# Kernel optimization log

Measured on AMD Instinct MI355X. Metric: run time of the kernel, lower is better.

Reference implementation:

```python
import jax, jax.numpy as jnp
import numpy as np

N = 100_000        # nodes
E = 1_600_000      # edges (avg degree 16)
IN_DIM = 256
OUT_DIM = 32
HEADS = 4
EDGE_DIM = 64
NUM_ETYPES = 8
NEG_SLOPE = 0.2


def setup_inputs() -> dict:
    key = jax.random.key(0)
    ks = jax.random.split(key, 12)
    h = jax.random.normal(ks[0], (N, IN_DIM), dtype=jnp.float32)
    row = jax.random.randint(ks[1], (E,), 0, N, dtype=jnp.int32)
    col = jax.random.randint(ks[2], (E,), 0, N, dtype=jnp.int32)
    etype = jax.random.randint(ks[3], (E,), 0, NUM_ETYPES, dtype=jnp.int32)
    # learned parameters (xavier-ish scale)
    W = jax.random.normal(ks[4], (IN_DIM, OUT_DIM * HEADS), dtype=jnp.float32) * 0.08
    edge_emb = jax.random.normal(ks[5], (NUM_ETYPES, EDGE_DIM), dtype=jnp.float32) * 0.2
    Wr = jax.random.normal(ks[6], (NUM_ETYPES, EDGE_DIM, EDGE_DIM * HEADS), dtype=jnp.float32) * 0.1
    a_l = jax.random.normal(ks[7], (1, HEADS, OUT_DIM), dtype=jnp.float32) * 0.3
    a_r = jax.random.normal(ks[8], (1, HEADS, OUT_DIM), dtype=jnp.float32) * 0.3
    a_e = jax.random.normal(ks[9], (1, HEADS, EDGE_DIM), dtype=jnp.float32) * 0.3
    res_W = jax.random.normal(ks[10], (IN_DIM, OUT_DIM * HEADS), dtype=jnp.float32) * 0.08
    res_b = jnp.zeros((OUT_DIM * HEADS,), dtype=jnp.float32)
    return dict(h=h, W=W, edge_emb=edge_emb, Wr=Wr, a_l=a_l, a_r=a_r, a_e=a_e,
                res_W=res_W, res_b=res_b, row=row, col=col, etype=etype)


def reference(h, W, edge_emb, Wr, a_l, a_r, a_e, res_W, res_b, row, col, etype):
    n = h.shape[0]
    heads, out_dim = a_l.shape[1], a_l.shape[2]
    edge_dim = a_e.shape[2]
    n_etypes = edge_emb.shape[0]

    # node transform: [N, H, D]
    emb = (h @ W).reshape(n, heads, out_dim)
    emb = jnp.where(jnp.isnan(emb), 0.0, emb)

    # typed linear on edge-type embeddings; only num_etypes distinct rows,
    # so compute per type then gather per edge (same math as W_r(edge_emb[etype]))
    e_trans = jnp.einsum('te,tef->tf', edge_emb, Wr).reshape(n_etypes, heads, edge_dim)
    h_e_type = (a_e * e_trans).sum(-1)            # [T, H]

    h_l = (a_l * emb).sum(-1)                     # [N, H]
    h_r = (a_r * emb).sum(-1)                     # [N, H]

    att = h_l[row] + h_r[col] + h_e_type[etype]   # [E, H]
    att = jnp.where(att > 0, att, NEG_SLOPE * att)  # leaky relu

    # edge softmax grouped by destination node (col)
    seg_max = jax.ops.segment_max(att, col, num_segments=n)   # [N, H]
    ex = jnp.exp(att - seg_max[col])
    seg_sum = jax.ops.segment_sum(ex, col, num_segments=n)    # [N, H]
    alpha = ex / seg_sum[col]                                  # [E, H]

    # u_mul_e + sum aggregation; emb permuted to [N, D, H] as in the original
    emb_p = emb.transpose(0, 2, 1)                 # [N, D, H]
    msg = emb_p[row] * alpha[:, None, :]           # [E, D, H]
    agg = jax.ops.segment_sum(msg, col, num_segments=n)  # [N, D, H]
    h_out = agg.reshape(n, out_dim * heads)

    h_out = h_out + h @ res_W + res_b              # residual linear
    return jax.nn.elu(h_out)
```

## Files before the change

### kernel.cpp

```cpp
#include <hip/hip_runtime.h>
#include <hip/hip_bf16.h>
#include <math.h>

#define N_NODES   100000
#define N_EDGES   1600000
#define IN_DIM    256
#define OUT_DIM   32
#define HEADS     4
#define C_DIM     128
#define EDGE_DIM  64
#define NUM_ETY   8
#define NEG_SLOPE 0.2f
#define NBLK_SCAN 391
#define M_TILE    128
#define BSTRIDE   40

typedef __attribute__((ext_vector_type(8))) short s8b;
typedef __attribute__((ext_vector_type(4))) float f32x4;
typedef unsigned short ushort_t;

__device__ __forceinline__ short bfc(float x) {
    __hip_bfloat16 b = __float2bfloat16(x);
    return *reinterpret_cast<short*>(&b);
}

__global__ void kz_init(unsigned int* __restrict__ counts) {
    int i = blockIdx.x * blockDim.x + threadIdx.x;
    if (i < N_NODES) counts[i] = 0u;
}

__global__ __launch_bounds__(256) void k_het(
    const float* __restrict__ edge_emb, const float* __restrict__ Wr,
    const float* __restrict__ a_e, float* __restrict__ h_et) {
    __shared__ float ee[EDGE_DIM];
    const int t = threadIdx.x;
    const int ty = blockIdx.x;
    if (t < EDGE_DIM) ee[t] = edge_emb[ty * EDGE_DIM + t];
    __syncthreads();
    const int hh = t >> 6, f = t & 63;
    float acc = 0.f;
#pragma unroll 8
    for (int e = 0; e < EDGE_DIM; ++e)
        acc += ee[e] * Wr[(size_t)(ty * EDGE_DIM + e) * (HEADS * EDGE_DIM) + hh * EDGE_DIM + f];
    acc *= a_e[hh * EDGE_DIM + f];
#pragma unroll
    for (int m = 32; m >= 1; m >>= 1) acc += __shfl_xor(acc, m);
    if (f == 0) h_et[ty * HEADS + hh] = acc;
}

__global__ void kw_prep(const float* __restrict__ W, const float* __restrict__ resW,
                        short* __restrict__ wt) {
    int idx = blockIdx.x * 256 + threadIdx.x;
    int k = idx >> 8, c = idx & 255;
    float v = (c < C_DIM) ? W[k * C_DIM + c] : resW[k * C_DIM + (c - C_DIM)];
    wt[c * IN_DIM + k] = bfc(v);
}

__global__ __launch_bounds__(512, 4) void k1_mfma(
    const float* __restrict__ h, const short* __restrict__ wt,
    const float* __restrict__ resb,
    const float* __restrict__ a_l, const float* __restrict__ a_r,
    ushort_t* __restrict__ embh, float* __restrict__ hl, float* __restrict__ hr,
    float* __restrict__ out) {
    __shared__ short bs[2][256 * BSTRIDE];
    const int t  = threadIdx.x;
    const int n0 = blockIdx.x * M_TILE;
    const int cstage = t >> 1, hstage = t & 1;

    {
        const s8b* src = (const s8b*)&wt[cstage * IN_DIM + hstage * 16];
        s8b v0 = src[0], v1 = src[1];
        *(s8b*)&bs[0][cstage * BSTRIDE + hstage * 16] = v0;
        *(s8b*)&bs[0][cstage * BSTRIDE + hstage * 16 + 8] = v1;
    }
    __syncthreads();

    const int lane = t & 63, w = t >> 6;
    const int wm = w >> 1;
    const int wn = w & 1;
    const int ln = lane & 15;
    const int kk = lane >> 4;

    const int gr0 = min(n0 + wm * 32 + ln, N_NODES - 1);
    const int gr1 = min(n0 + wm * 32 + 16 + ln, N_NODES - 1);
    const float* __restrict__ ha0 = &h[(size_t)gr0 * IN_DIM + kk * 8];
    const float* __restrict__ ha1 = &h[(size_t)gr1 * IN_DIM + kk * 8];

    f32x4 acc[2][8];
#pragma unroll
    for (int mf = 0; mf < 2; ++mf)
#pragma unroll
        for (int nf = 0; nf < 8; ++nf) acc[mf][nf] = (f32x4){0.f, 0.f, 0.f, 0.f};

    int cur = 0;
#pragma unroll
    for (int ks = 0; ks < 8; ++ks) {
        s8b nb0 = {}, nb1 = {};
        if (ks < 7) {
            const s8b* src = (const s8b*)&wt[cstage * IN_DIM + (ks + 1) * 32 + hstage * 16];
            nb0 = src[0];
            nb1 = src[1];
        }

        float4 l0 = *(const float4*)&ha0[ks * 32];
        float4 h0 = *(const float4*)&ha0[ks * 32 + 4];
        float4 l1 = *(const float4*)&ha1[ks * 32];
        float4 h1 = *(const float4*)&ha1[ks * 32 + 4];
        s8b a0, a1;
        a0[0] = bfc(l0.x); a0[1] = bfc(l0.y); a0[2] = bfc(l0.z); a0[3] = bfc(l0.w);
        a0[4] = bfc(h0.x); a0[5] = bfc(h0.y); a0[6] = bfc(h0.z); a0[7] = bfc(h0.w);
        a1[0] = bfc(l1.x); a1[1] = bfc(l1.y); a1[2] = bfc(l1.z); a1[3] = bfc(l1.w);
        a1[4] = bfc(h1.x); a1[5] = bfc(h1.y); a1[6] = bfc(h1.z); a1[7] = bfc(h1.w);

#pragma unroll
        for (int nf = 0; nf < 8; ++nf) {
            int c = wn * 128 + nf * 16 + ln;
            s8b b = *(const s8b*)&bs[cur][c * BSTRIDE + kk * 8];
            acc[0][nf] = __builtin_amdgcn_mfma_f32_16x16x32_bf16(a0, b, acc[0][nf], 0, 0, 0);
            acc[1][nf] = __builtin_amdgcn_mfma_f32_16x16x32_bf16(a1, b, acc[1][nf], 0, 0, 0);
        }

        if (ks < 7) {
            *(s8b*)&bs[cur ^ 1][cstage * BSTRIDE + hstage * 16] = nb0;
            *(s8b*)&bs[cur ^ 1][cstage * BSTRIDE + hstage * 16 + 8] = nb1;
        }
        __syncthreads();
        cur ^= 1;
    }

    if (wn == 0) {
#pragma unroll
        for (int mf = 0; mf < 2; ++mf)
#pragma unroll
            for (int nf = 0; nf < 8; ++nf) {
                int col = nf * 16 + ln;
#pragma unroll
                for (int r = 0; r < 4; ++r) {
                    int nd = n0 + wm * 32 + mf * 16 + kk * 4 + r;
                    if (nd < N_NODES)
                        embh[(size_t)nd * C_DIM + col] = (ushort_t)bfc(acc[mf][nf][r]);
                }
            }
#pragma unroll
        for (int mf = 0; mf < 2; ++mf)
#pragma unroll
            for (int hh = 0; hh < HEADS; ++hh) {
                float al0 = a_l[hh * 32 + ln], al1 = a_l[hh * 32 + 16 + ln];
                float ar0 = a_r[hh * 32 + ln], ar1 = a_r[hh * 32 + 16 + ln];
#pragma unroll
                for (int r = 0; r < 4; ++r) {
                    float pl = al0 * acc[mf][2 * hh][r] + al1 * acc[mf][2 * hh + 1][r];
                    float pr = ar0 * acc[mf][2 * hh][r] + ar1 * acc[mf][2 * hh + 1][r];
#pragma unroll
                    for (int m = 8; m >= 1; m >>= 1) {
                        pl += __shfl_xor(pl, m);
                        pr += __shfl_xor(pr, m);
                    }
                    int nd = n0 + wm * 32 + mf * 16 + kk * 4 + r;
                    if (ln == 0 && nd < N_NODES) {
                        hl[nd * HEADS + hh] = pl;
                        hr[nd * HEADS + hh] = pr;
                    }
                }
            }
    } else {
#pragma unroll
        for (int mf = 0; mf < 2; ++mf)
#pragma unroll
            for (int nf = 0; nf < 8; ++nf) {
                int col = nf * 16 + ln;
                float rb = resb[col];
#pragma unroll
                for (int r = 0; r < 4; ++r) {
                    int nd = n0 + wm * 32 + mf * 16 + kk * 4 + r;
                    if (nd < N_NODES) out[(size_t)nd * C_DIM + col] = acc[mf][nf][r] + rb;
                }
            }
    }
}

__global__ void b1_hist(const int* __restrict__ col, unsigned int* __restrict__ counts) {
    int e = blockIdx.x * blockDim.x + threadIdx.x;
    if (e < N_EDGES) atomicAdd(&counts[col[e]], 1u);
}

__global__ __launch_bounds__(256) void bscan1(const unsigned int* __restrict__ counts,
                                              unsigned int* __restrict__ offs,
                                              unsigned int* __restrict__ bsum) {
    __shared__ unsigned int s[256];
    int t = threadIdx.x;
    int g = blockIdx.x * 256 + t;
    unsigned int v = (g < N_NODES) ? counts[g] : 0u;
    s[t] = v;
    __syncthreads();
    for (int off = 1; off < 256; off <<= 1) {
        unsigned int x = (t >= off) ? s[t - off] : 0u;
        __syncthreads();
        s[t] += x;
        __syncthreads();
    }
    if (g < N_NODES) offs[g] = s[t] - v;
    if (t == 255) bsum[blockIdx.x] = s[255];
}

__global__ __launch_bounds__(512) void bscan2(unsigned int* __restrict__ bsum) {
    __shared__ unsigned int s[512];
    int t = threadIdx.x;
    unsigned int v = (t < NBLK_SCAN) ? bsum[t] : 0u;
    s[t] = v;
    __syncthreads();
    for (int off = 1; off < 512; off <<= 1) {
        unsigned int x = (t >= off) ? s[t - off] : 0u;
        __syncthreads();
        s[t] += x;
        __syncthreads();
    }
    if (t < NBLK_SCAN) bsum[t] = s[t] - v;
}

__global__ void bscan3(unsigned int* __restrict__ offs, const unsigned int* __restrict__ bsum,
                       unsigned int* __restrict__ cursor) {
    int g = blockIdx.x * blockDim.x + threadIdx.x;
    if (g < N_NODES) {
        unsigned int o = offs[g] + bsum[g >> 8];
        offs[g] = o;
        cursor[g] = o;
    }
    if (g == 0) offs[N_NODES] = N_EDGES;
}

__global__ void b4_scatter(const int* __restrict__ row, const int* __restrict__ col,
                           const int* __restrict__ ety,
                           const float* __restrict__ hl, const float* __restrict__ hr,
                           const float* __restrict__ het,
                           unsigned int* __restrict__ cursor,
                           float4* __restrict__ plog, int* __restrict__ prow) {
    int e = blockIdx.x * blockDim.x + threadIdx.x;
    if (e >= N_EDGES) return;
    int r = row[e], c = col[e], ty = ety[e];
    unsigned int pos = atomicAdd(&cursor[c], 1u);
    float4 l  = *(const float4*)&hl[r * 4];
    float4 rr = *(const float4*)&hr[c * 4];
    float4 te = *(const float4*)&het[ty * 4];
    float a0 = l.x + rr.x + te.x;
    float a1 = l.y + rr.y + te.y;
    float a2 = l.z + rr.z + te.z;
    float a3 = l.w + rr.w + te.w;
    a0 = a0 > 0.f ? a0 : NEG_SLOPE * a0;
    a1 = a1 > 0.f ? a1 : NEG_SLOPE * a1;
    a2 = a2 > 0.f ? a2 : NEG_SLOPE * a2;
    a3 = a3 > 0.f ? a3 : NEG_SLOPE * a3;
    plog[pos] = make_float4(a0, a1, a2, a3);
    prow[pos] = r;
}

__device__ __forceinline__ void online_upd(float& m, float& s, float l) {
    float nm = fmaxf(m, l);
    s = s * __expf(m - nm) + __expf(l - nm);
    m = nm;
}

__global__ __launch_bounds__(256) void k_fused(
    const unsigned int* __restrict__ offs, const float4* __restrict__ plog,
    const int* __restrict__ prow, const ushort_t* __restrict__ embh,
    float* __restrict__ out) {
    __shared__ float alds[4][16][4];
    __shared__ int   rlds[4][16];
    const int w    = threadIdx.x >> 6;
    const int lane = threadIdx.x & 63;
    const int c    = blockIdx.x * 4 + w;
    if (c >= N_NODES) return;

    const unsigned int start = offs[c], end = offs[c + 1];

    float m0 = -1e30f, m1 = -1e30f, m2 = -1e30f, m3 = -1e30f;
    float s0 = 0.f, s1 = 0.f, s2 = 0.f, s3 = 0.f;
    for (unsigned int i = start + lane; i < end; i += 64) {
        float4 L = plog[i];
        online_upd(m0, s0, L.x);
        online_upd(m1, s1, L.y);
        online_upd(m2, s2, L.z);
        online_upd(m3, s3, L.w);
    }
#pragma unroll
    for (int off = 32; off >= 1; off >>= 1) {
        float mo, so, nm;
        mo = __shfl_xor(m0, off); so = __shfl_xor(s0, off);
        nm = fmaxf(m0, mo); s0 = s0 * __expf(m0 - nm) + so * __expf(mo - nm); m0 = nm;
        mo = __shfl_xor(m1, off); so = __shfl_xor(s1, off);
        nm = fmaxf(m1, mo); s1 = s1 * __expf(m1 - nm) + so * __expf(mo - nm); m1 = nm;
        mo = __shfl_xor(m2, off); so = __shfl_xor(s2, off);
        nm = fmaxf(m2, mo); s2 = s2 * __expf(m2 - nm) + so * __expf(mo - nm); m2 = nm;
        mo = __shfl_xor(m3, off); so = __shfl_xor(s3, off);
        nm = fmaxf(m3, mo); s3 = s3 * __expf(m3 - nm) + so * __expf(mo - nm); m3 = nm;
    }
    const bool hasE = end > start;
    const float i0 = hasE ? 1.f / s0 : 0.f;
    const float i1 = hasE ? 1.f / s1 : 0.f;
    const float i2 = hasE ? 1.f / s2 : 0.f;
    const float i3 = hasE ? 1.f / s3 : 0.f;

    const int hd = lane >> 4;
    float accA = 0.f, accB = 0.f;

    for (unsigned int base = start; base < end; base += 16) {
        int cnt = (int)min(16u, end - base);
        if (lane < cnt) {
            float4 L = plog[base + lane];
            alds[w][lane][0] = __expf(L.x - m0) * i0;
            alds[w][lane][1] = __expf(L.y - m1) * i1;
            alds[w][lane][2] = __expf(L.z - m2) * i2;
            alds[w][lane][3] = __expf(L.w - m3) * i3;
            rlds[w][lane] = prow[base + lane];
        }
        for (int j = 0; j < cnt; ++j) {
            int r = rlds[w][j];
            float al = alds[w][j][hd];
            unsigned int v = *(const unsigned int*)&embh[(size_t)r * C_DIM + lane * 2];
            float lo = __uint_as_float(v << 16);
            float hi = __uint_as_float(v & 0xffff0000u);
            accA = fmaf(al, lo, accA);
            accB = fmaf(al, hi, accB);
        }
    }

    const int d  = (2 * lane) & 31;
    const int oA = d * 4 + hd;
    const int oB = oA + 4;
    size_t ob = (size_t)c * C_DIM;
    float x0 = out[ob + oA] + accA;
    float x1 = out[ob + oB] + accB;
    out[ob + oA] = x0 > 0.f ? x0 : expm1f(x0);
    out[ob + oB] = x1 > 0.f ? x1 : expm1f(x1);
}

extern "C" void kernel_launch(void* const* d_in, const int* in_sizes, int n_in,
                              void* d_out, int out_size, void* d_ws, size_t ws_size,
                              hipStream_t stream) {
    const float* h        = (const float*)d_in[0];
    const float* W        = (const float*)d_in[1];
    const float* edge_emb = (const float*)d_in[2];
    const float* Wr       = (const float*)d_in[3];
    const float* a_l      = (const float*)d_in[4];
    const float* a_r      = (const float*)d_in[5];
    const float* a_e      = (const float*)d_in[6];
    const float* res_W    = (const float*)d_in[7];
    const float* res_b    = (const float*)d_in[8];
    const int*   row      = (const int*)d_in[9];
    const int*   col      = (const int*)d_in[10];
    const int*   etype    = (const int*)d_in[11];
    float* out = (float*)d_out;

    float* ws = (float*)d_ws;
    float4*       ws_plog  = (float4*)ws;
    float*        p        = ws + (size_t)N_EDGES * 4;
    ushort_t*     ws_embh  = (ushort_t*)p;
    p += (size_t)N_NODES * C_DIM / 2;
    float*        ws_hl    = p;  p += (size_t)N_NODES * HEADS;
    float*        ws_hr    = p;  p += (size_t)N_NODES * HEADS;
    float*        ws_het   = p;  p += 32;
    unsigned int* ws_offs  = (unsigned int*)p;
    unsigned int* ws_cur   = ws_offs + (N_NODES + 1);
    unsigned int* ws_cnt   = ws_cur + N_NODES;
    unsigned int* ws_bsum  = ws_cnt + N_NODES;
    int*          ws_prow  = (int*)(ws_bsum + NBLK_SCAN);
    short*        ws_wt    = (short*)(ws_prow + N_EDGES);

    kz_init<<<(N_NODES + 255) / 256, 256, 0, stream>>>(ws_cnt);

    k_het<<<NUM_ETY, 256, 0, stream>>>(edge_emb, Wr, a_e, ws_het);

    kw_prep<<<256, 256, 0, stream>>>(W, res_W, ws_wt);

    k1_mfma<<<(N_NODES + M_TILE - 1) / M_TILE, 512, 0, stream>>>(
        h, ws_wt, res_b, a_l, a_r, ws_embh, ws_hl, ws_hr, out);

    b1_hist<<<(N_EDGES + 255) / 256, 256, 0, stream>>>(col, ws_cnt);

    bscan1<<<NBLK_SCAN, 256, 0, stream>>>(ws_cnt, ws_offs, ws_bsum);
    bscan2<<<1, 512, 0, stream>>>(ws_bsum);
    bscan3<<<(N_NODES + 255) / 256, 256, 0, stream>>>(ws_offs, ws_bsum, ws_cur);

    b4_scatter<<<(N_EDGES + 255) / 256, 256, 0, stream>>>(
        row, col, etype, ws_hl, ws_hr, ws_het, ws_cur, ws_plog, ws_prow);

    k_fused<<<(N_NODES + 3) / 4, 256, 0, stream>>>(
        ws_offs, ws_plog, ws_prow, ws_embh, out);
}
```

Before: 530.8 us.

## Halve k1_mfma block to 256 threads with 64-row per-wave tiles

The node-transform GEMM kernel now runs 4 waves per block instead of 8, and each wave computes four 16-row M fragments instead of two. Each B fragment read from shared memory is therefore reused across more MFMAs, and each thread stages a full 32-element B row slice per k-step. The cost is a larger accumulator set (128 floats per lane), which raises register pressure, and fewer waves are available to hide global-load latency on h.

```diff
diff --git a/kernel.cpp b/kernel.cpp
--- a/kernel.cpp
+++ b/kernel.cpp
@@ -56,7 +56,7 @@
     wt[c * IN_DIM + k] = bfc(v);
 }
 
-__global__ __launch_bounds__(512, 4) void k1_mfma(
+__global__ __launch_bounds__(256, 2) void k1_mfma(
     const float* __restrict__ h, const short* __restrict__ wt,
     const float* __restrict__ resb,
     const float* __restrict__ a_l, const float* __restrict__ a_r,
@@ -65,13 +65,13 @@
     __shared__ short bs[2][256 * BSTRIDE];
     const int t  = threadIdx.x;
     const int n0 = blockIdx.x * M_TILE;
-    const int cstage = t >> 1, hstage = t & 1;
 
     {
-        const s8b* src = (const s8b*)&wt[cstage * IN_DIM + hstage * 16];
-        s8b v0 = src[0], v1 = src[1];
-        *(s8b*)&bs[0][cstage * BSTRIDE + hstage * 16] = v0;
-        *(s8b*)&bs[0][cstage * BSTRIDE + hstage * 16 + 8] = v1;
+#pragma unroll
+        for (int j = 0; j < 4; ++j) {
+            s8b v = *(const s8b*)&wt[t * IN_DIM + j * 8];
+            *(s8b*)&bs[0][t * BSTRIDE + j * 8] = v;
+        }
     }
     __syncthreads();
 
@@ -81,48 +81,58 @@
     const int ln = lane & 15;
     const int kk = lane >> 4;
 
-    const int gr0 = min(n0 + wm * 32 + ln, N_NODES - 1);
-    const int gr1 = min(n0 + wm * 32 + 16 + ln, N_NODES - 1);
-    const float* __restrict__ ha0 = &h[(size_t)gr0 * IN_DIM + kk * 8];
-    const float* __restrict__ ha1 = &h[(size_t)gr1 * IN_DIM + kk * 8];
-
-    f32x4 acc[2][8];
-#pragma unroll
-    for (int mf = 0; mf < 2; ++mf)
+    const float* __restrict__ ha[4];
+#pragma unroll
+    for (int mf = 0; mf < 4; ++mf) {
+        int gr = min(n0 + wm * 64 + mf * 16 + ln, N_NODES - 1);
+        ha[mf] = &h[(size_t)gr * IN_DIM + kk * 8];
+    }
+
+    f32x4 acc[4][8];
+#pragma unroll
+    for (int mf = 0; mf < 4; ++mf)
 #pragma unroll
         for (int nf = 0; nf < 8; ++nf) acc[mf][nf] = (f32x4){0.f, 0.f, 0.f, 0.f};
 
     int cur = 0;
 #pragma unroll
     for (int ks = 0; ks < 8; ++ks) {
-        s8b nb0 = {}, nb1 = {};
+        s8b nb0 = {}, nb1 = {}, nb2 = {}, nb3 = {};
         if (ks < 7) {
-            const s8b* src = (const s8b*)&wt[cstage * IN_DIM + (ks + 1) * 32 + hstage * 16];
-            nb0 = src[0];
-            nb1 = src[1];
-        }
-
-        float4 l0 = *(const float4*)&ha0[ks * 32];
-        float4 h0 = *(const float4*)&ha0[ks * 32 + 4];
-        float4 l1 = *(const float4*)&ha1[ks * 32];
-        float4 h1 = *(const float4*)&ha1[ks * 32 + 4];
-        s8b a0, a1;
-        a0[0] = bfc(l0.x); a0[1] = bfc(l0.y); a0[2] = bfc(l0.z); a0[3] = bfc(l0.w);
-        a0[4] = bfc(h0.x); a0[5] = bfc(h0.y); a0[6] = bfc(h0.z); a0[7] = bfc(h0.w);
-        a1[0] = bfc(l1.x); a1[1] = bfc(l1.y); a1[2] = bfc(l1.z); a1[3] = bfc(l1.w);
-        a1[4] = bfc(h1.x); a1[5] = bfc(h1.y); a1[6] = bfc(h1.z); a1[7] = bfc(h1.w);
+            const short* src = &wt[t * IN_DIM + (ks + 1) * 32];
+            nb0 = *(const s8b*)&src[0];
+            nb1 = *(const s8b*)&src[8];
+            nb2 = *(const s8b*)&src[16];
+            nb3 = *(const s8b*)&src[24];
+        }
+
+        s8b a[4];
+#pragma unroll
+        for (int mf = 0; mf < 4; ++mf) {
+            float4 lo = *(const float4*)&ha[mf][ks * 32];
+            float4 hi = *(const float4*)&ha[mf][ks * 32 + 4];
+            a[mf][0] = bfc(lo.x); a[mf][1] = bfc(lo.y);
+            a[mf][2] = bfc(lo.z); a[mf][3] = bfc(lo.w);
+            a[mf][4] = bfc(hi.x); a[mf][5] = bfc(hi.y);
+            a[mf][6] = bfc(hi.z); a[mf][7] = bfc(hi.w);
+        }
 
 #pragma unroll
         for (int nf = 0; nf < 8; ++nf) {
             int c = wn * 128 + nf * 16 + ln;
             s8b b = *(const s8b*)&bs[cur][c * BSTRIDE + kk * 8];
-            acc[0][nf] = __builtin_amdgcn_mfma_f32_16x16x32_bf16(a0, b, acc[0][nf], 0, 0, 0);
-            acc[1][nf] = __builtin_amdgcn_mfma_f32_16x16x32_bf16(a1, b, acc[1][nf], 0, 0, 0);
+            acc[0][nf] = __builtin_amdgcn_mfma_f32_16x16x32_bf16(a[0], b, acc[0][nf], 0, 0, 0);
+            acc[1][nf] = __builtin_amdgcn_mfma_f32_16x16x32_bf16(a[1], b, acc[1][nf], 0, 0, 0);
+            acc[2][nf] = __builtin_amdgcn_mfma_f32_16x16x32_bf16(a[2], b, acc[2][nf], 0, 0, 0);
+            acc[3][nf] = __builtin_amdgcn_mfma_f32_16x16x32_bf16(a[3], b, acc[3][nf], 0, 0, 0);
         }
 
         if (ks < 7) {
-            *(s8b*)&bs[cur ^ 1][cstage * BSTRIDE + hstage * 16] = nb0;
-            *(s8b*)&bs[cur ^ 1][cstage * BSTRIDE + hstage * 16 + 8] = nb1;
+            short* dst = &bs[cur ^ 1][t * BSTRIDE];
+            *(s8b*)&dst[0]  = nb0;
+            *(s8b*)&dst[8]  = nb1;
+            *(s8b*)&dst[16] = nb2;
+            *(s8b*)&dst[24] = nb3;
         }
         __syncthreads();
         cur ^= 1;
@@ -130,19 +140,19 @@
 
     if (wn == 0) {
 #pragma unroll
-        for (int mf = 0; mf < 2; ++mf)
+        for (int mf = 0; mf < 4; ++mf)
 #pragma unroll
             for (int nf = 0; nf < 8; ++nf) {
                 int col = nf * 16 + ln;
 #pragma unroll
                 for (int r = 0; r < 4; ++r) {
-                    int nd = n0 + wm * 32 + mf * 16 + kk * 4 + r;
+                    int nd = n0 + wm * 64 + mf * 16 + kk * 4 + r;
                     if (nd < N_NODES)
                         embh[(size_t)nd * C_DIM + col] = (ushort_t)bfc(acc[mf][nf][r]);
                 }
             }
 #pragma unroll
-        for (int mf = 0; mf < 2; ++mf)
+        for (int mf = 0; mf < 4; ++mf)
 #pragma unroll
             for (int hh = 0; hh < HEADS; ++hh) {
                 float al0 = a_l[hh * 32 + ln], al1 = a_l[hh * 32 + 16 + ln];
@@ -156,7 +166,7 @@
                         pl += __shfl_xor(pl, m);
                         pr += __shfl_xor(pr, m);
                     }
-                    int nd = n0 + wm * 32 + mf * 16 + kk * 4 + r;
+                    int nd = n0 + wm * 64 + mf * 16 + kk * 4 + r;
                     if (ln == 0 && nd < N_NODES) {
                         hl[nd * HEADS + hh] = pl;
                         hr[nd * HEADS + hh] = pr;
@@ -165,14 +175,14 @@
             }
     } else {
 #pragma unroll
-        for (int mf = 0; mf < 2; ++mf)
+        for (int mf = 0; mf < 4; ++mf)
 #pragma unroll
             for (int nf = 0; nf < 8; ++nf) {
                 int col = nf * 16 + ln;
                 float rb = resb[col];
 #pragma unroll
                 for (int r = 0; r < 4; ++r) {
-                    int nd = n0 + wm * 32 + mf * 16 + kk * 4 + r;
+                    int nd = n0 + wm * 64 + mf * 16 + kk * 4 + r;
                     if (nd < N_NODES) out[(size_t)nd * C_DIM + col] = acc[mf][nf][r] + rb;
                 }
             }
@@ -372,7 +382,7 @@
 
     kw_prep<<<256, 256, 0, stream>>>(W, res_W, ws_wt);
 
-    k1_mfma<<<(N_NODES + M_TILE - 1) / M_TILE, 512, 0, stream>>>(
+    k1_mfma<<<(N_NODES + M_TILE - 1) / M_TILE, 256, 0, stream>>>(
         h, ws_wt, res_b, a_l, a_r, ws_embh, ws_hl, ws_hr, out);
 
     b1_hist<<<(N_EDGES + 255) / 256, 256, 0, stream>>>(col, ws_cnt);
```

New measurement: 529.1 us. About the same (-0.3%).
